# Optimization experiments

Measured on AMD Instinct MI355X. Metric: run time of the kernel, lower is better.

## Reference

```python
import jax, jax.numpy as jnp
import numpy as np

B, S, D, H = 16, 2048, 2048, 16
HD = D // H
PROJ = D  # proj_ratio = 1.0
PAD_ID = 50257
LN_EPS = 1e-5
MASKED_BIAS = -1e9


def setup_inputs() -> dict:
    key = jax.random.key(0)
    ks = jax.random.split(key, 12)
    sc = 0.02
    return {
        "hidden_states": jax.random.normal(ks[0], (B, S, D), dtype=jnp.float32),
        "input_ids_with_pads": jax.random.randint(ks[1], (B, S), 0, PAD_ID, dtype=jnp.int64),
        "ln_w": jnp.ones((D,), jnp.float32),
        "ln_b": jnp.zeros((D,), jnp.float32),
        "wq": sc * jax.random.normal(ks[2], (D, D), jnp.float32),
        "bq": jnp.zeros((D,), jnp.float32),
        "wk": sc * jax.random.normal(ks[3], (D, D), jnp.float32),
        "bk": jnp.zeros((D,), jnp.float32),
        "wv": sc * jax.random.normal(ks[4], (D, D), jnp.float32),
        "bv": jnp.zeros((D,), jnp.float32),
        "wo": sc * jax.random.normal(ks[5], (D, PROJ), jnp.float32),
        "bo": jnp.zeros((PROJ,), jnp.float32),
    }


def _layernorm(x, g, b):
    mu = jnp.mean(x, axis=-1, keepdims=True)
    var = jnp.mean(jnp.square(x - mu), axis=-1, keepdims=True)
    return (x - mu) * jax.lax.rsqrt(var + LN_EPS) * g + b


def _last_token_index(tokens):
    # select_at_last_token: argmax of cumsum of the non-pad mask == index of
    # the last non-pad token (first index where the cumsum reaches its max).
    mask = (tokens != PAD_ID).astype(jnp.int32)
    return jnp.argmax(jnp.cumsum(mask, axis=1), axis=1)  # [B]


def reference(hidden_states, input_ids_with_pads, ln_w, ln_b,
              wq, bq, wk, bk, wv, bv, wo, bo):
    x = _layernorm(hidden_states, ln_w, ln_b)  # [B,S,D]
    idx = _last_token_index(input_ids_with_pads)
    # Efficient gather instead of the original index_select + diagonal trick.
    x_last = x[jnp.arange(B), idx]  # [B,D]

    q = (x_last @ wq + bq).reshape(B, H, HD)          # single query per batch
    k = (x @ wk + bk).reshape(B, S, H, HD).transpose(0, 2, 1, 3)  # [B,H,S,HD]
    v = (x @ wv + bv).reshape(B, S, H, HD).transpose(0, 2, 1, 3)  # [B,H,S,HD]

    # GPT-Neo _attn: compute in float32, NO 1/sqrt(head_dim) scaling.
    # Causal mask for query at position key_length-1 covers the full key range,
    # i.e. it is all-True here, so it is a no-op (kept implicit).
    w = jnp.einsum("bhd,bhsd->bhs", q.astype(jnp.float32), k.astype(jnp.float32))
    w = jax.nn.softmax(w, axis=-1).astype(v.dtype)    # [B,H,S]
    attn = jnp.einsum("bhs,bhsd->bhd", w, v)          # [B,H,HD]
    attn = attn.reshape(B, D)                          # merge heads
    out = attn @ wo + bo                               # [B,PROJ]
    return out
```

## Files before the change

### kernel.cpp

```cpp
#include <hip/hip_runtime.h>
#include <hip/hip_bf16.h>

#define BB 16
#define SS 2048
#define DD 2048
#define HH 16
#define HDIM 128
#define PAD_ID 50257
#define LN_EPS 1e-5f

__device__ __forceinline__ float block_sum256(float v, float* s4) {
    #pragma unroll
    for (int m = 32; m >= 1; m >>= 1) v += __shfl_xor(v, m, 64);
    __syncthreads();
    if ((threadIdx.x & 63) == 0) s4[threadIdx.x >> 6] = v;
    __syncthreads();
    return s4[0] + s4[1] + s4[2] + s4[3];
}
__device__ __forceinline__ float block_max256(float v, float* s4) {
    #pragma unroll
    for (int m = 32; m >= 1; m >>= 1) v = fmaxf(v, __shfl_xor(v, m, 64));
    __syncthreads();
    if ((threadIdx.x & 63) == 0) s4[threadIdx.x >> 6] = v;
    __syncthreads();
    return fmaxf(fmaxf(s4[0], s4[1]), fmaxf(s4[2], s4[3]));
}

__device__ __forceinline__ void gl16(const float* g, float* l) {
    __builtin_amdgcn_global_load_lds(
        (const __attribute__((address_space(1))) void*)g,
        (__attribute__((address_space(3))) void*)l,
        16, 0, 0);
}

__global__ __launch_bounds__(256) void k_prep(const float* __restrict__ hid, const int* __restrict__ ids,
                                              const float* __restrict__ g, const float* __restrict__ be,
                                              float* __restrict__ xlast) {
    int b = blockIdx.x, t = threadIdx.x;
    __shared__ int sm[256];
    __shared__ float s4[4];
    const int* row = ids + (size_t)b * SS;
    int best = -1;
    for (int s = t; s < SS; s += 256)
        if (row[s] != PAD_ID) best = s;
    sm[t] = best;
    __syncthreads();
    for (int off = 128; off > 0; off >>= 1) {
        if (t < off) sm[t] = max(sm[t], sm[t + off]);
        __syncthreads();
    }
    int idx = (sm[0] < 0) ? 0 : sm[0];
    const float4* row4 = (const float4*)(hid + ((size_t)b * SS + idx) * DD);
    float4 v0 = row4[t], v1 = row4[t + 256];
    float s  = v0.x + v0.y + v0.z + v0.w + v1.x + v1.y + v1.z + v1.w;
    float sq = v0.x*v0.x + v0.y*v0.y + v0.z*v0.z + v0.w*v0.w
             + v1.x*v1.x + v1.y*v1.y + v1.z*v1.z + v1.w*v1.w;
    s  = block_sum256(s, s4);
    sq = block_sum256(sq, s4);
    float mu = s * (1.0f / DD);
    float rstd = rsqrtf(sq * (1.0f / DD) - mu * mu + LN_EPS);
    const float4* g4 = (const float4*)g;
    const float4* b4 = (const float4*)be;
    float4 ga = g4[t], gb = g4[t + 256], ba = b4[t], bb = b4[t + 256];
    float4 o0, o1;
    o0.x = (v0.x - mu) * rstd * ga.x + ba.x;  o0.y = (v0.y - mu) * rstd * ga.y + ba.y;
    o0.z = (v0.z - mu) * rstd * ga.z + ba.z;  o0.w = (v0.w - mu) * rstd * ga.w + ba.w;
    o1.x = (v1.x - mu) * rstd * gb.x + bb.x;  o1.y = (v1.y - mu) * rstd * gb.y + bb.y;
    o1.z = (v1.z - mu) * rstd * gb.z + bb.z;  o1.w = (v1.w - mu) * rstd * gb.w + bb.w;
    ((float4*)(xlast + (size_t)b * DD))[t]       = o0;
    ((float4*)(xlast + (size_t)b * DD))[t + 256] = o1;
}

__global__ __launch_bounds__(256) void k_init3(float* __restrict__ q, float* __restrict__ attn,
                                               float* __restrict__ out, const float* __restrict__ bq,
                                               const float* __restrict__ bv, const float* __restrict__ bo) {
    int i = blockIdx.x * 256 + threadIdx.x;
    int which = blockIdx.y;
    float* dst = which == 0 ? q : (which == 1 ? attn : out);
    const float* bias = which == 0 ? bq : (which == 1 ? bv : bo);
    dst[i] = bias[i & (DD - 1)];
}

__global__ __launch_bounds__(256) void k_q(const float* __restrict__ xlast, const float* __restrict__ wq,
                                           float* __restrict__ q) {
    int ptile = blockIdx.x, kch = blockIdx.y, tid = threadIdx.x;
    __shared__ float xs[16][64];
    {
        int b = tid >> 4, c4 = tid & 15;
        *(float4*)&xs[b][c4 * 4] = *(const float4*)&xlast[(size_t)b * DD + kch * 64 + c4 * 4];
    }
    __syncthreads();
    int p = ptile * 256 + tid;
    float acc[16];
    #pragma unroll
    for (int b = 0; b < 16; b++) acc[b] = 0.f;
    for (int dd = 0; dd < 64; dd++) {
        float wqv = wq[(size_t)(kch * 64 + dd) * DD + p];
        #pragma unroll
        for (int b = 0; b < 16; b++) acc[b] = fmaf(xs[b][dd], wqv, acc[b]);
    }
    #pragma unroll
    for (int b = 0; b < 16; b++) atomicAdd(&q[(size_t)b * DD + p], acc[b]);
}

__global__ __launch_bounds__(256) void k_t(const float* __restrict__ wk, const float* __restrict__ q,
                                           const float* __restrict__ g, float* __restrict__ t_out,
                                           float* __restrict__ tg_out) {
    int d = blockIdx.x, tid = threadIdx.x;
    __shared__ float wkl[16 * 132];
    #pragma unroll
    for (int k = 0; k < 2; k++) {
        int f4 = tid + k * 256;
        int h = f4 >> 5, j4 = f4 & 31;
        *(float4*)&wkl[h * 132 + j4 * 4] = *(const float4*)&wk[(size_t)d * DD + h * 128 + j4 * 4];
    }
    __syncthreads();
    int b = tid >> 4, h = tid & 15;
    const float4* q4 = (const float4*)(q + (size_t)b * DD + h * 128);
    float acc = 0.f;
    #pragma unroll
    for (int j4 = 0; j4 < 32; j4++) {
        float4 qv = q4[j4];
        float4 wv4 = *(const float4*)&wkl[h * 132 + j4 * 4];
        acc = fmaf(qv.x, wv4.x, fmaf(qv.y, wv4.y, fmaf(qv.z, wv4.z, fmaf(qv.w, wv4.w, acc))));
    }
    size_t o = (size_t)(b * 16 + h) * DD + d;
    t_out[o] = acc;
    tg_out[o] = acc * g[d];
}

__global__ __launch_bounds__(256) void k_G(const float* __restrict__ t_in, const float* __restrict__ tg_in,
                                           const float* __restrict__ q, const float* __restrict__ lnb,
                                           const float* __restrict__ bk, float* __restrict__ G1,
                                           float* __restrict__ wconst) {
    int bh = blockIdx.x, tid = threadIdx.x;
    int b = bh >> 4, h = bh & 15;
    __shared__ float s4[4];
    const float4* tg4 = (const float4*)(tg_in + (size_t)bh * DD);
    const float4* t4  = (const float4*)(t_in + (size_t)bh * DD);
    const float4* lb4 = (const float4*)lnb;
    float g1p = 0.f, g2p = 0.f;
    #pragma unroll
    for (int k = 0; k < 2; k++) {
        int f = tid + k * 256;
        float4 a = tg4[f];
        g1p += a.x + a.y + a.z + a.w;
        float4 tv = t4[f];
        float4 bv = lb4[f];
        g2p = fmaf(tv.x, bv.x, fmaf(tv.y, bv.y, fmaf(tv.z, bv.z, fmaf(tv.w, bv.w, g2p))));
    }
    float cp = 0.f;
    if (tid < 128) cp = bk[h * 128 + tid] * q[(size_t)b * DD + h * 128 + tid];
    float G1v = block_sum256(g1p, s4);
    float rest = block_sum256(g2p + cp, s4);
    if (tid == 0) { G1[bh] = G1v; wconst[bh] = rest; }
}

__global__ __launch_bounds__(256) void k_logits8(const float* __restrict__ hid, const float* __restrict__ tg,
                                                 const float* __restrict__ G1, const float* __restrict__ wcst,
                                                 float* __restrict__ wout, float* __restrict__ muA,
                                                 float* __restrict__ rsA) {
    __shared__ float smem[12288];
    int b = blockIdx.x, st = blockIdx.y;
    int tid = threadIdx.x, qd = tid & 15, rp = tid >> 4;
    const float* hb = hid + ((size_t)b * SS + st * 32) * DD;
    const float* tgb = tg + (size_t)b * 16 * DD;

    float raw[2][16], sum[2], ssq[2];
    #pragma unroll
    for (int r = 0; r < 2; r++) {
        sum[r] = 0.f; ssq[r] = 0.f;
        #pragma unroll
        for (int h = 0; h < 16; h++) raw[r][h] = 0.f;
    }

    auto stage = [&](int c, int buf) {
        int d0 = c * 128;
        float* xd = smem + buf * 4096;
        float* td = smem + 8192 + buf * 2048;
        #pragma unroll
        for (int i = 0; i < 4; i++) {
            int f = i * 256 + tid;
            int row = f >> 5, c4 = f & 31;
            gl16(&hb[(size_t)row * DD + d0 + c4 * 4], &xd[f * 4]);
        }
        #pragma unroll
        for (int i = 0; i < 2; i++) {
            int f = i * 256 + tid;
            int h = f >> 5, c4 = f & 31;
            gl16(&tgb[(size_t)h * DD + d0 + c4 * 4], &td[f * 4]);
        }
    };

    stage(0, 0);
    __syncthreads();

    int cur = 0;
    #pragma unroll 1
    for (int c = 0; c < 16; c++) {
        if (c < 15) stage(c + 1, cur ^ 1);
        const float* xb = smem + cur * 4096;
        const float* tb = smem + 8192 + cur * 2048;
        #pragma unroll
        for (int k = 0; k < 2; k++) {
            float4 x0 = *(const float4*)&xb[(rp * 2 + 0) * 128 + (qd + 16 * k) * 4];
            float4 x1 = *(const float4*)&xb[(rp * 2 + 1) * 128 + (qd + 16 * k) * 4];
            #pragma unroll
            for (int h = 0; h < 16; h++) {
                float4 tv = *(const float4*)&tb[h * 128 + (qd + 16 * k) * 4];
                raw[0][h] = fmaf(x0.x, tv.x, fmaf(x0.y, tv.y, fmaf(x0.z, tv.z, fmaf(x0.w, tv.w, raw[0][h]))));
                raw[1][h] = fmaf(x1.x, tv.x, fmaf(x1.y, tv.y, fmaf(x1.z, tv.z, fmaf(x1.w, tv.w, raw[1][h]))));
            }
            sum[0] += x0.x + x0.y + x0.z + x0.w;
            sum[1] += x1.x + x1.y + x1.z + x1.w;
            ssq[0] = fmaf(x0.x, x0.x, fmaf(x0.y, x0.y, fmaf(x0.z, x0.z, fmaf(x0.w, x0.w, ssq[0]))));
            ssq[1] = fmaf(x1.x, x1.x, fmaf(x1.y, x1.y, fmaf(x1.z, x1.z, fmaf(x1.w, x1.w, ssq[1]))));
        }
        __syncthreads();
        cur ^= 1;
    }

    #pragma unroll
    for (int m = 1; m < 16; m <<= 1) {
        #pragma unroll
        for (int r = 0; r < 2; r++) {
            sum[r] += __shfl_xor(sum[r], m, 64);
            ssq[r] += __shfl_xor(ssq[r], m, 64);
        }
    }

    float g1 = G1[b * 16 + qd];
    float wc = wcst[b * 16 + qd];
    float* red = smem;
    #pragma unroll
    for (int rr = 0; rr < 2; rr++) {
        __syncthreads();
        #pragma unroll
        for (int h = 0; h < 16; h++) red[tid * 17 + h] = raw[rr][h];
        __syncthreads();
        float tot = 0.f;
        #pragma unroll
        for (int j = 0; j < 16; j++) tot += red[(rp * 16 + j) * 17 + qd];
        int s = st * 32 + rp * 2 + rr;
        float mu = sum[rr] * (1.0f / DD);
        float rstd = rsqrtf(ssq[rr] * (1.0f / DD) - mu * mu + LN_EPS);
        wout[(size_t)(b * 16 + qd) * SS + s] = rstd * (tot - mu * g1) + wc;
        if (qd == 0) { muA[(size_t)b * SS + s] = mu; rsA[(size_t)b * SS + s] = rstd; }
    }
}

__global__ __launch_bounds__(256) void k_softmax(const float* __restrict__ wlog, const float* __restrict__ muA,
                                                 const float* __restrict__ rsA, float* __restrict__ coef,
                                                 float* __restrict__ Mout) {
    int bh = blockIdx.x, tid = threadIdx.x;
    int b = bh >> 4;
    __shared__ float s4[4];
    const float4* w4 = (const float4*)(wlog + (size_t)bh * SS);
    float4 v0 = w4[tid], v1 = w4[tid + 256];
    float mx = fmaxf(fmaxf(fmaxf(v0.x, v0.y), fmaxf(v0.z, v0.w)),
                     fmaxf(fmaxf(v1.x, v1.y), fmaxf(v1.z, v1.w)));
    mx = block_max256(mx, s4);
    float4 e0, e1;
    e0.x = __expf(v0.x - mx); e0.y = __expf(v0.y - mx); e0.z = __expf(v0.z - mx); e0.w = __expf(v0.w - mx);
    e1.x = __expf(v1.x - mx); e1.y = __expf(v1.y - mx); e1.z = __expf(v1.z - mx); e1.w = __expf(v1.w - mx);
    float ssum = e0.x + e0.y + e0.z + e0.w + e1.x + e1.y + e1.z + e1.w;
    ssum = block_sum256(ssum, s4);
    float inv = 1.0f / ssum;
    const float4* r4 = (const float4*)(rsA + (size_t)b * SS);
    const float4* m4 = (const float4*)(muA + (size_t)b * SS);
    float4 ra = r4[tid], rb = r4[tid + 256], ma = m4[tid], mb = m4[tid + 256];
    float4 c0, c1;
    c0.x = e0.x * inv * ra.x; c0.y = e0.y * inv * ra.y; c0.z = e0.z * inv * ra.z; c0.w = e0.w * inv * ra.w;
    c1.x = e1.x * inv * rb.x; c1.y = e1.y * inv * rb.y; c1.z = e1.z * inv * rb.z; c1.w = e1.w * inv * rb.w;
    ((float4*)(coef + (size_t)bh * SS))[tid] = c0;
    ((float4*)(coef + (size_t)bh * SS))[tid + 256] = c1;
    float Mp = c0.x * ma.x + c0.y * ma.y + c0.z * ma.z + c0.w * ma.w
             + c1.x * mb.x + c1.y * mb.y + c1.z * mb.z + c1.w * mb.w;
    Mp = block_sum256(Mp, s4);
    if (tid == 0) Mout[bh] = Mp;
}

__global__ __launch_bounds__(256) void k_pv6(const float* __restrict__ hid, const float* __restrict__ coef,
                                             float* __restrict__ Apart) {
    int b = blockIdx.x, dt = blockIdx.y, ch = blockIdx.z, tid = threadIdx.x;
    __shared__ float cl[128][16];
    int s0 = ch * 128;
    #pragma unroll
    for (int k = 0; k < 2; k++) {
        int f = tid + k * 256; int h = f >> 5, s4i = f & 31;
        float4 c4 = *(const float4*)&coef[(size_t)(b * 16 + h) * SS + s0 + s4i * 4];
        cl[s4i * 4 + 0][h] = c4.x; cl[s4i * 4 + 1][h] = c4.y;
        cl[s4i * 4 + 2][h] = c4.z; cl[s4i * 4 + 3][h] = c4.w;
    }
    __syncthreads();
    int d = dt * 1024 + tid * 4;
    const float* hb = hid + ((size_t)b * SS + s0) * DD + d;
    float4 acc[16];
    #pragma unroll
    for (int h = 0; h < 16; h++) acc[h] = make_float4(0.f, 0.f, 0.f, 0.f);
    float4 xv[8];
    #pragma unroll
    for (int i = 0; i < 8; i++) xv[i] = *(const float4*)(hb + (size_t)i * DD);
    #pragma unroll 1
    for (int sb = 0; sb < 16; sb++) {
        #pragma unroll
        for (int i = 0; i < 8; i++) {
            int s = sb * 8 + i;
            float4 x = xv[i];
            if (sb < 15) xv[i] = *(const float4*)(hb + (size_t)(s + 8) * DD);
            float4 ca = *(const float4*)&cl[s][0];
            float4 cb = *(const float4*)&cl[s][4];
            float4 cc = *(const float4*)&cl[s][8];
            float4 cd = *(const float4*)&cl[s][12];
            acc[0].x = fmaf(ca.x, x.x, acc[0].x); acc[0].y = fmaf(ca.x, x.y, acc[0].y);
            acc[0].z = fmaf(ca.x, x.z, acc[0].z); acc[0].w = fmaf(ca.x, x.w, acc[0].w);
            acc[1].x = fmaf(ca.y, x.x, acc[1].x); acc[1].y = fmaf(ca.y, x.y, acc[1].y);
            acc[1].z = fmaf(ca.y, x.z, acc[1].z); acc[1].w = fmaf(ca.y, x.w, acc[1].w);
            acc[2].x = fmaf(ca.z, x.x, acc[2].x); acc[2].y = fmaf(ca.z, x.y, acc[2].y);
            acc[2].z = fmaf(ca.z, x.z, acc[2].z); acc[2].w = fmaf(ca.z, x.w, acc[2].w);
            acc[3].x = fmaf(ca.w, x.x, acc[3].x); acc[3].y = fmaf(ca.w, x.y, acc[3].y);
            acc[3].z = fmaf(ca.w, x.z, acc[3].z); acc[3].w = fmaf(ca.w, x.w, acc[3].w);
            acc[4].x = fmaf(cb.x, x.x, acc[4].x); acc[4].y = fmaf(cb.x, x.y, acc[4].y);
            acc[4].z = fmaf(cb.x, x.z, acc[4].z); acc[4].w = fmaf(cb.x, x.w, acc[4].w);
            acc[5].x = fmaf(cb.y, x.x, acc[5].x); acc[5].y = fmaf(cb.y, x.y, acc[5].y);
            acc[5].z = fmaf(cb.y, x.z, acc[5].z); acc[5].w = fmaf(cb.y, x.w, acc[5].w);
            acc[6].x = fmaf(cb.z, x.x, acc[6].x); acc[6].y = fmaf(cb.z, x.y, acc[6].y);
            acc[6].z = fmaf(cb.z, x.z, acc[6].z); acc[6].w = fmaf(cb.z, x.w, acc[6].w);
            acc[7].x = fmaf(cb.w, x.x, acc[7].x); acc[7].y = fmaf(cb.w, x.y, acc[7].y);
            acc[7].z = fmaf(cb.w, x.z, acc[7].z); acc[7].w = fmaf(cb.w, x.w, acc[7].w);
            acc[8].x = fmaf(cc.x, x.x, acc[8].x); acc[8].y = fmaf(cc.x, x.y, acc[8].y);
            acc[8].z = fmaf(cc.x, x.z, acc[8].z); acc[8].w = fmaf(cc.x, x.w, acc[8].w);
            acc[9].x = fmaf(cc.y, x.x, acc[9].x); acc[9].y = fmaf(cc.y, x.y, acc[9].y);
            acc[9].z = fmaf(cc.y, x.z, acc[9].z); acc[9].w = fmaf(cc.y, x.w, acc[9].w);
            acc[10].x = fmaf(cc.z, x.x, acc[10].x); acc[10].y = fmaf(cc.z, x.y, acc[10].y);
            acc[10].z = fmaf(cc.z, x.z, acc[10].z); acc[10].w = fmaf(cc.z, x.w, acc[10].w);
            acc[11].x = fmaf(cc.w, x.x, acc[11].x); acc[11].y = fmaf(cc.w, x.y, acc[11].y);
            acc[11].z = fmaf(cc.w, x.z, acc[11].z); acc[11].w = fmaf(cc.w, x.w, acc[11].w);
            acc[12].x = fmaf(cd.x, x.x, acc[12].x); acc[12].y = fmaf(cd.x, x.y, acc[12].y);
            acc[12].z = fmaf(cd.x, x.z, acc[12].z); acc[12].w = fmaf(cd.x, x.w, acc[12].w);
            acc[13].x = fmaf(cd.y, x.x, acc[13].x); acc[13].y = fmaf(cd.y, x.y, acc[13].y);
            acc[13].z = fmaf(cd.y, x.z, acc[13].z); acc[13].w = fmaf(cd.y, x.w, acc[13].w);
            acc[14].x = fmaf(cd.z, x.x, acc[14].x); acc[14].y = fmaf(cd.z, x.y, acc[14].y);
            acc[14].z = fmaf(cd.z, x.z, acc[14].z); acc[14].w = fmaf(cd.z, x.w, acc[14].w);
            acc[15].x = fmaf(cd.w, x.x, acc[15].x); acc[15].y = fmaf(cd.w, x.y, acc[15].y);
            acc[15].z = fmaf(cd.w, x.z, acc[15].z); acc[15].w = fmaf(cd.w, x.w, acc[15].w);
        }
    }
    #pragma unroll
    for (int h = 0; h < 16; h++)
        *(float4*)&Apart[((size_t)(ch * 16 + b) * 16 + h) * DD + d] = acc[h];
}

__global__ __launch_bounds__(256) void k_red(const float* __restrict__ Apart, float* __restrict__ A) {
    size_t i4 = (size_t)blockIdx.x * 256 + threadIdx.x;
    const float4* ap = (const float4*)Apart;
    float4 acc = make_float4(0.f, 0.f, 0.f, 0.f);
    #pragma unroll
    for (int c = 0; c < 16; c++) {
        float4 v = ap[(size_t)c * 131072 + i4];
        acc.x += v.x; acc.y += v.y; acc.z += v.z; acc.w += v.w;
    }
    ((float4*)A)[i4] = acc;
}

__global__ __launch_bounds__(256) void k_attnv(const float* __restrict__ A, const float* __restrict__ M,
                                               const float* __restrict__ g, const float* __restrict__ be,
                                               const float* __restrict__ wv, float* __restrict__ attn) {
    int h = blockIdx.x, dc = blockIdx.y, tid = threadIdx.x;
    __shared__ float yl[16][64];
    int d0 = dc * 64;
    {
        int b = tid >> 4, c4 = tid & 15;
        float4 a4 = *(const float4*)&A[(size_t)(b * 16 + h) * DD + d0 + c4 * 4];
        float4 g4 = *(const float4*)&g[d0 + c4 * 4];
        float4 b4 = *(const float4*)&be[d0 + c4 * 4];
        float m = M[b * 16 + h];
        float4 y;
        y.x = g4.x * (a4.x - m) + b4.x;  y.y = g4.y * (a4.y - m) + b4.y;
        y.z = g4.z * (a4.z - m) + b4.z;  y.w = g4.w * (a4.w - m) + b4.w;
        *(float4*)&yl[b][c4 * 4] = y;
    }
    __syncthreads();
    int j = tid & 127, h2 = tid >> 7;
    float acc[16];
    #pragma unroll
    for (int b = 0; b < 16; b++) acc[b] = 0.f;
    for (int dl = 0; dl < 32; dl++) {
        int dd = h2 * 32 + dl;
        float wvv = wv[(size_t)(d0 + dd) * DD + h * 128 + j];
        #pragma unroll
        for (int b = 0; b < 16; b++) acc[b] = fmaf(yl[b][dd], wvv, acc[b]);
    }
    #pragma unroll
    for (int b = 0; b < 16; b++) atomicAdd(&attn[(size_t)b * DD + h * 128 + j], acc[b]);
}

__global__ __launch_bounds__(256) void k_out(const float* __restrict__ attn, const float* __restrict__ wo,
                                             float* __restrict__ out) {
    int ptile = blockIdx.x, cch = blockIdx.y, tid = threadIdx.x;
    __shared__ float al[16][64];
    int c0 = cch * 64;
    {
        int b = tid >> 4, c4 = tid & 15;
        *(float4*)&al[b][c4 * 4] = *(const float4*)&attn[(size_t)b * DD + c0 + c4 * 4];
    }
    __syncthreads();
    int p = ptile * 256 + tid;
    float acc[16];
    #pragma unroll
    for (int b = 0; b < 16; b++) acc[b] = 0.f;
    for (int cc = 0; cc < 64; cc++) {
        float wov = wo[(size_t)(c0 + cc) * DD + p];
        #pragma unroll
        for (int b = 0; b < 16; b++) acc[b] = fmaf(al[b][cc], wov, acc[b]);
    }
    #pragma unroll
    for (int b = 0; b < 16; b++) atomicAdd(&out[(size_t)b * DD + p], acc[b]);
}

extern "C" void kernel_launch(void* const* d_in, const int* in_sizes, int n_in,
                              void* d_out, int out_size, void* d_ws, size_t ws_size,
                              hipStream_t stream) {
    const float* hid = (const float*)d_in[0];
    const int*   ids = (const int*)d_in[1];
    const float* lnw = (const float*)d_in[2];
    const float* lnb = (const float*)d_in[3];
    const float* wq  = (const float*)d_in[4];
    const float* bq  = (const float*)d_in[5];
    const float* wk  = (const float*)d_in[6];
    const float* bk  = (const float*)d_in[7];
    const float* wv  = (const float*)d_in[8];
    const float* bv  = (const float*)d_in[9];
    const float* wo  = (const float*)d_in[10];
    const float* bo  = (const float*)d_in[11];
    float* out = (float*)d_out;

    float* ws = (float*)d_ws;
    float* xlast = ws;
    float* q     = xlast + 32768;
    float* t     = q + 32768;
    float* tg    = t + 524288;
    float* G1    = tg + 524288;
    float* wcst  = G1 + 256;
    float* wlog  = wcst + 256;
    float* muA   = wlog + 524288;
    float* rsA   = muA + 32768;
    float* coef  = rsA + 32768;
    float* Mbh   = coef + 524288;
    float* Abh   = Mbh + 256;
    float* attn  = Abh + 524288;
    float* Apart = attn + 32768;

    k_prep<<<16, 256, 0, stream>>>(hid, ids, lnw, lnb, xlast);
    k_init3<<<dim3(128, 3), 256, 0, stream>>>(q, attn, out, bq, bv, bo);
    k_q<<<dim3(8, 32), 256, 0, stream>>>(xlast, wq, q);
    k_t<<<2048, 256, 0, stream>>>(wk, q, lnw, t, tg);
    k_G<<<256, 256, 0, stream>>>(t, tg, q, lnb, bk, G1, wcst);
    k_logits8<<<dim3(16, 64), 256, 0, stream>>>(hid, tg, G1, wcst, wlog, muA, rsA);
    k_softmax<<<256, 256, 0, stream>>>(wlog, muA, rsA, coef, Mbh);
    k_pv6<<<dim3(16, 2, 16), 256, 0, stream>>>(hid, coef, Apart);
    k_red<<<512, 256, 0, stream>>>(Apart, Abh);
    k_attnv<<<dim3(16, 32), 256, 0, stream>>>(Abh, Mbh, lnw, lnb, wv, attn);
    k_out<<<dim3(8, 32), 256, 0, stream>>>(attn, wo, out);
}
```

Baseline: 227.1 us.

## Triple-buffer logits kernel with smaller chunks and vmcnt-based waits

Reworks the logits kernel's shared-memory pipeline. It goes from double buffering 128-wide chunks with a full syncthreads to triple buffering 64-wide chunks that are prefetched two stages ahead. It waits with explicit s_waitcnt vmcnt plus a raw barrier, so loads stay in flight across iterations, and shared memory drops from 48KB to 36KB, which could raise occupancy. The risk is that the hand-counted vmcnt is wrong, or that the extra barriers per chunk add overhead.

```diff
diff --git a/kernel.cpp b/kernel.cpp
--- a/kernel.cpp
+++ b/kernel.cpp
@@ -156,11 +156,11 @@
     if (tid == 0) { G1[bh] = G1v; wconst[bh] = rest; }
 }
 
-__global__ __launch_bounds__(256) void k_logits8(const float* __restrict__ hid, const float* __restrict__ tg,
-                                                 const float* __restrict__ G1, const float* __restrict__ wcst,
-                                                 float* __restrict__ wout, float* __restrict__ muA,
-                                                 float* __restrict__ rsA) {
-    __shared__ float smem[12288];
+__global__ __launch_bounds__(256) void k_logits10(const float* __restrict__ hid, const float* __restrict__ tg,
+                                                  const float* __restrict__ G1, const float* __restrict__ wcst,
+                                                  float* __restrict__ wout, float* __restrict__ muA,
+                                                  float* __restrict__ rsA) {
+    __shared__ float smem[9216];
     int b = blockIdx.x, st = blockIdx.y;
     int tid = threadIdx.x, qd = tid & 15, rp = tid >> 4;
     const float* hb = hid + ((size_t)b * SS + st * 32) * DD;
@@ -175,49 +175,51 @@
     }
 
     auto stage = [&](int c, int buf) {
-        int d0 = c * 128;
-        float* xd = smem + buf * 4096;
-        float* td = smem + 8192 + buf * 2048;
-        #pragma unroll
-        for (int i = 0; i < 4; i++) {
-            int f = i * 256 + tid;
-            int row = f >> 5, c4 = f & 31;
-            gl16(&hb[(size_t)row * DD + d0 + c4 * 4], &xd[f * 4]);
-        }
+        int d0 = c * 64;
+        float* xd = smem + buf * 2048;
+        float* td = smem + 6144 + buf * 1024;
         #pragma unroll
         for (int i = 0; i < 2; i++) {
             int f = i * 256 + tid;
-            int h = f >> 5, c4 = f & 31;
-            gl16(&tgb[(size_t)h * DD + d0 + c4 * 4], &td[f * 4]);
+            int row = f >> 4, c4 = f & 15;
+            gl16(&hb[(size_t)row * DD + d0 + c4 * 4], &xd[f * 4]);
+        }
+        {
+            int h = tid >> 4, c4 = tid & 15;
+            gl16(&tgb[(size_t)h * DD + d0 + c4 * 4], &smem[6144 + buf * 1024 + tid * 4]);
+            (void)td;
         }
     };
 
     stage(0, 0);
-    __syncthreads();
-
-    int cur = 0;
+    stage(1, 1);
+
+    int cb = 0;
     #pragma unroll 1
-    for (int c = 0; c < 16; c++) {
-        if (c < 15) stage(c + 1, cur ^ 1);
-        const float* xb = smem + cur * 4096;
-        const float* tb = smem + 8192 + cur * 2048;
-        #pragma unroll
-        for (int k = 0; k < 2; k++) {
-            float4 x0 = *(const float4*)&xb[(rp * 2 + 0) * 128 + (qd + 16 * k) * 4];
-            float4 x1 = *(const float4*)&xb[(rp * 2 + 1) * 128 + (qd + 16 * k) * 4];
-            #pragma unroll
-            for (int h = 0; h < 16; h++) {
-                float4 tv = *(const float4*)&tb[h * 128 + (qd + 16 * k) * 4];
-                raw[0][h] = fmaf(x0.x, tv.x, fmaf(x0.y, tv.y, fmaf(x0.z, tv.z, fmaf(x0.w, tv.w, raw[0][h]))));
-                raw[1][h] = fmaf(x1.x, tv.x, fmaf(x1.y, tv.y, fmaf(x1.z, tv.z, fmaf(x1.w, tv.w, raw[1][h]))));
-            }
-            sum[0] += x0.x + x0.y + x0.z + x0.w;
-            sum[1] += x1.x + x1.y + x1.z + x1.w;
-            ssq[0] = fmaf(x0.x, x0.x, fmaf(x0.y, x0.y, fmaf(x0.z, x0.z, fmaf(x0.w, x0.w, ssq[0]))));
-            ssq[1] = fmaf(x1.x, x1.x, fmaf(x1.y, x1.y, fmaf(x1.z, x1.z, fmaf(x1.w, x1.w, ssq[1]))));
-        }
-        __syncthreads();
-        cur ^= 1;
+    for (int c = 0; c < 32; c++) {
+        if (c < 31) { asm volatile("s_waitcnt vmcnt(3)" ::: "memory"); }
+        else        { asm volatile("s_waitcnt vmcnt(0)" ::: "memory"); }
+        __builtin_amdgcn_s_barrier();
+        asm volatile("" ::: "memory");
+        if (c + 2 < 32) {
+            int sb = cb + 2; if (sb >= 3) sb -= 3;
+            stage(c + 2, sb);
+        }
+        const float* xb = smem + cb * 2048;
+        const float* tb = smem + 6144 + cb * 1024;
+        float4 x0 = *(const float4*)&xb[(rp * 2 + 0) * 64 + qd * 4];
+        float4 x1 = *(const float4*)&xb[(rp * 2 + 1) * 64 + qd * 4];
+        #pragma unroll
+        for (int h = 0; h < 16; h++) {
+            float4 tv = *(const float4*)&tb[h * 64 + qd * 4];
+            raw[0][h] = fmaf(x0.x, tv.x, fmaf(x0.y, tv.y, fmaf(x0.z, tv.z, fmaf(x0.w, tv.w, raw[0][h]))));
+            raw[1][h] = fmaf(x1.x, tv.x, fmaf(x1.y, tv.y, fmaf(x1.z, tv.z, fmaf(x1.w, tv.w, raw[1][h]))));
+        }
+        sum[0] += x0.x + x0.y + x0.z + x0.w;
+        sum[1] += x1.x + x1.y + x1.z + x1.w;
+        ssq[0] = fmaf(x0.x, x0.x, fmaf(x0.y, x0.y, fmaf(x0.z, x0.z, fmaf(x0.w, x0.w, ssq[0]))));
+        ssq[1] = fmaf(x1.x, x1.x, fmaf(x1.y, x1.y, fmaf(x1.z, x1.z, fmaf(x1.w, x1.w, ssq[1]))));
+        cb = cb + 1; if (cb >= 3) cb -= 3;
     }
 
     #pragma unroll
@@ -377,7 +379,7 @@
         float m = M[b * 16 + h];
         float4 y;
         y.x = g4.x * (a4.x - m) + b4.x;  y.y = g4.y * (a4.y - m) + b4.y;
-        y.z = g4.z * (a4.z - m) + b4.z;  y.w = g4.w * (a4.w - m) + b4.w;
+    	y.z = g4.z * (a4.z - m) + b4.z;  y.w = g4.w * (a4.w - m) + b4.w;
         *(float4*)&yl[b][c4 * 4] = y;
     }
     __syncthreads();
@@ -456,7 +458,7 @@
     k_q<<<dim3(8, 32), 256, 0, stream>>>(xlast, wq, q);
     k_t<<<2048, 256, 0, stream>>>(wk, q, lnw, t, tg);
     k_G<<<256, 256, 0, stream>>>(t, tg, q, lnb, bk, G1, wcst);
-    k_logits8<<<dim3(16, 64), 256, 0, stream>>>(hid, tg, G1, wcst, wlog, muA, rsA);
+    k_logits10<<<dim3(16, 64), 256, 0, stream>>>(hid, tg, G1, wcst, wlog, muA, rsA);
     k_softmax<<<256, 256, 0, stream>>>(wlog, muA, rsA, coef, Mbh);
     k_pv6<<<dim3(16, 2, 16), 256, 0, stream>>>(hid, coef, Apart);
     k_red<<<512, 256, 0, stream>>>(Apart, Abh);
```

Result: slower. 243.2 us (+7.1%).
